# Kernel optimization log

Measured on AMD Instinct MI355X. Metric: run time of the kernel, lower is better.

Reference implementation:

```python
import jax, jax.numpy as jnp
import numpy as np

B = 8192
G, K, D = 8, 1024, 64  # num_codebooks, codebook_size, code_dim
INIT_SCALE = 0.1


def setup_inputs() -> dict:
    key = jax.random.key(0)
    kz, kc = jax.random.split(key)
    z = jax.random.normal(kz, (B, G * D), dtype=jnp.float32)
    codebook = jax.random.uniform(kc, (G, K, D), dtype=jnp.float32,
                                  minval=-INIT_SCALE, maxval=INIT_SCALE)
    return {"z": z, "codebook": codebook}


def reference(z, codebook):
    # Eval-mode forward of GroupedVectorQuantizer (no EMA buffer mutation).
    b = z.shape[0]
    g, k, d = codebook.shape
    zg = z.reshape(b, g, d)                       # [B,G,D]
    # squared L2 distance via ||z||^2 + ||c||^2 - 2 z.c (avoids [B,G,K,D] diff tensor)
    z2 = jnp.sum(zg * zg, axis=-1, keepdims=True)           # [B,G,1]
    c2 = jnp.sum(codebook * codebook, axis=-1)[None]        # [1,G,K]
    zc = jnp.einsum('bgd,gkd->bgk', zg, codebook)           # [B,G,K]
    dist = z2 + c2 - 2.0 * zc                               # [B,G,K]
    indices = jnp.argmin(dist, axis=-1)                     # [B,G] int32
    # gather nearest codes per group
    zq = codebook[jnp.arange(g)[None, :], indices]          # [B,G,D]
    commitment_loss = jnp.mean((zg - jax.lax.stop_gradient(zq)) ** 2)
    codebook_loss = jnp.zeros((), dtype=z.dtype)
    # straight-through estimator
    z_st = zg + jax.lax.stop_gradient(zq - zg)
    quantized_flat = z_st.reshape(b, g * d)
    # codebook usage entropy / perplexity (pooled over batch and groups, as in torch)
    usage = jnp.zeros((k,), dtype=jnp.float32).at[indices.reshape(-1)].add(1.0) / (b * g)
    entropy = -jnp.sum(usage * jnp.log(usage + 1e-10))
    perplexity = jnp.exp(entropy)
    return quantized_flat, indices, commitment_loss, codebook_loss, entropy, perplexity
```

## Files before the change

kernel.cpp:

```cpp
#include <hip/hip_runtime.h>
#include <hip/hip_bf16.h>
#include <math.h>

#define NB 8192
#define NG 8
#define NK 1024
#define ND 64
#define GD 512
#define MARGIN 2.5e-4f

typedef __attribute__((ext_vector_type(8))) short short8;
typedef __attribute__((ext_vector_type(4))) float f32x4;

#define WS_C2_OFF   0
#define WS_STG_OFF  32768
#define WS_HIST_OFF (32768 + 2097152 + 1048576)
#define WS_PART_OFF (WS_HIST_OFF + 4096)

typedef const __attribute__((address_space(1))) unsigned int glds_src_t;
typedef __attribute__((address_space(3))) unsigned int glds_dst_t;

__device__ inline void bsplit(float v, short& hs, short& ls) {
    __hip_bfloat16 h = __float2bfloat16(v);
    float hf = __bfloat162float(h);
    __hip_bfloat16 l = __float2bfloat16(v - hf);
    hs = *reinterpret_cast<short*>(&h);
    ls = *reinterpret_cast<short*>(&l);
}

__device__ inline float wredsum(float v) {
#pragma unroll
    for (int st = 1; st < 64; st <<= 1) v += __shfl_xor(v, st);
    return v;
}

__global__ __launch_bounds__(64) void vq_prep(const float* __restrict__ cb,
                                              float* __restrict__ ws) {
    const int gid = blockIdx.x * 64 + threadIdx.x;
    const int g  = gid >> 10, k = gid & 1023;
    const int it = k >> 6,   row = k & 63;
    const float* c = cb + (size_t)gid * ND;
    char* base = (char*)ws + WS_STG_OFF + (size_t)(g * 16 + it) * 16384 + row * 128;

    float a0 = 0.f, a1 = 0.f, a2 = 0.f, a3 = 0.f;
#pragma unroll
    for (int j = 0; j < 8; ++j) {
        const float4 v0 = reinterpret_cast<const float4*>(c)[2 * j];
        const float4 v1 = reinterpret_cast<const float4*>(c)[2 * j + 1];
        a0 = fmaf(v0.x, v0.x, a0); a1 = fmaf(v0.y, v0.y, a1);
        a2 = fmaf(v0.z, v0.z, a2); a3 = fmaf(v0.w, v0.w, a3);
        a0 = fmaf(v1.x, v1.x, a0); a1 = fmaf(v1.y, v1.y, a1);
        a2 = fmaf(v1.z, v1.z, a2); a3 = fmaf(v1.w, v1.w, a3);
        short h0, l0, h1, l1, h2, l2, h3, l3;
        short h4, l4, h5, l5, h6, l6, h7, l7;
        bsplit(v0.x, h0, l0); bsplit(v0.y, h1, l1);
        bsplit(v0.z, h2, l2); bsplit(v0.w, h3, l3);
        bsplit(v1.x, h4, l4); bsplit(v1.y, h5, l5);
        bsplit(v1.z, h6, l6); bsplit(v1.w, h7, l7);
        short8 hs, ls;
        hs[0] = h0; hs[1] = h1; hs[2] = h2; hs[3] = h3;
        hs[4] = h4; hs[5] = h5; hs[6] = h6; hs[7] = h7;
        ls[0] = l0; ls[1] = l1; ls[2] = l2; ls[3] = l3;
        ls[4] = l4; ls[5] = l5; ls[6] = l6; ls[7] = l7;
        const int off = (j ^ (row & 7)) << 4;
        *reinterpret_cast<short8*>(base + off)        = hs;
        *reinterpret_cast<short8*>(base + 8192 + off) = ls;
    }
    ((float*)((char*)ws + WS_C2_OFF))[gid] = (a0 + a1) + (a2 + a3);
    if (gid < NK) ((unsigned*)((char*)ws + WS_HIST_OFF))[gid] = 0u;
}

__global__ __launch_bounds__(256, 2) void vq_score(const float* __restrict__ z,
                                                   const float* __restrict__ cb,
                                                   float* __restrict__ out,
                                                   float* __restrict__ ws) {
    __shared__ __align__(16) char smem[2][32768];
    __shared__ int winfo[4][32];
    const int tid  = threadIdx.x;
    const int w    = tid >> 6;
    const int lane = tid & 63;
    const int lo   = lane & 15, hi = lane >> 4;
    const int g    = blockIdx.y;
    const int rbase = blockIdx.x * 128 + w * 32;

    const char*  stg = (const char*)ws + WS_STG_OFF + (size_t)g * 16 * 16384;
    const float* c2g = (const float*)((const char*)ws + WS_C2_OFF) + g * NK;

    short8 Ah[2][2], Al[2][2];
#pragma unroll
    for (int m = 0; m < 2; ++m)
#pragma unroll
        for (int ks = 0; ks < 2; ++ks) {
            const float* zp = z + (size_t)(rbase + m * 16 + lo) * GD + g * ND + ks * 32 + hi * 8;
            float vv[8];
            *reinterpret_cast<float4*>(&vv[0]) = reinterpret_cast<const float4*>(zp)[0];
            *reinterpret_cast<float4*>(&vv[4]) = reinterpret_cast<const float4*>(zp)[1];
#pragma unroll
            for (int e = 0; e < 8; ++e) {
                short hs, ls;
                bsplit(vv[e], hs, ls);
                Ah[m][ks][e] = hs;
                Al[m][ks][e] = ls;
            }
        }

    float best[8], b2[8];
    int   bk[8], k2[8];
#pragma unroll
    for (int s = 0; s < 8; ++s) { best[s] = 3.0e38f; b2[s] = 3.0e38f; bk[s] = 0; k2[s] = 0; }

    const int rowoff = lo * 128;
    const int swz0 = ((hi ^ (lo & 7)) << 4);
    const int swz1 = (((4 + hi) ^ (lo & 7)) << 4);
    char* lds0 = &smem[0][0];

    const char* src = stg;
    auto STAGE = [&](const char* s, unsigned dOff) {
#pragma unroll
        for (int i = 0; i < 8; ++i) {
            const int so = (i >> 2) * 16384 + w * 4096 + (i & 3) * 1024 + lane * 16;
            __builtin_amdgcn_global_load_lds(
                (glds_src_t*)(const void*)(s + so),
                (glds_dst_t*)(void*)(lds0 + dOff + so), 16, 0, 0);
        }
    };

    STAGE(src, 0u);
    src += 32768;
    __syncthreads();

#pragma unroll 1
    for (int it = 0; it < 8; ++it) {
        float c2v[2][4];
#pragma unroll
        for (int t = 0; t < 2; ++t)
#pragma unroll
            for (int n = 0; n < 4; ++n)
                c2v[t][n] = c2g[it * 128 + t * 64 + n * 16 + lo];

        const unsigned cur = (unsigned)(it & 1) * 32768u;
        if (it < 7) { STAGE(src, cur ^ 32768u); src += 32768; }

        const char* bufc = lds0 + cur;
#pragma unroll
        for (int t = 0; t < 2; ++t) {
            f32x4 acc[2][4] = {};
#pragma unroll
            for (int ks = 0; ks < 2; ++ks) {
                short8 bh[4], bl[4];
#pragma unroll
                for (int n = 0; n < 4; ++n) {
                    const int off = t * 16384 + n * 2048 + rowoff + (ks ? swz1 : swz0);
                    bh[n] = *reinterpret_cast<const short8*>(bufc + off);
                    bl[n] = *reinterpret_cast<const short8*>(bufc + 8192 + off);
                }
#pragma unroll
                for (int n = 0; n < 4; ++n)
#pragma unroll
                    for (int m = 0; m < 2; ++m)
                        acc[m][n] = __builtin_amdgcn_mfma_f32_16x16x32_bf16(
                            ks ? Ah[m][1] : Ah[m][0], bh[n], acc[m][n], 0, 0, 0);
#pragma unroll
                for (int n = 0; n < 4; ++n)
#pragma unroll
                    for (int m = 0; m < 2; ++m)
                        acc[m][n] = __builtin_amdgcn_mfma_f32_16x16x32_bf16(
                            ks ? Ah[m][1] : Ah[m][0], bl[n], acc[m][n], 0, 0, 0);
#pragma unroll
                for (int n = 0; n < 4; ++n)
#pragma unroll
                    for (int m = 0; m < 2; ++m)
                        acc[m][n] = __builtin_amdgcn_mfma_f32_16x16x32_bf16(
                            ks ? Al[m][1] : Al[m][0], bh[n], acc[m][n], 0, 0, 0);
            }

#pragma unroll
            for (int n = 0; n < 4; ++n) {
                const int kv = it * 128 + t * 64 + n * 16 + lo;
#pragma unroll
                for (int m = 0; m < 2; ++m)
#pragma unroll
                    for (int q = 0; q < 4; ++q) {
                        const int sidx = m * 4 + q;
                        const float s = fmaf(-2.0f, acc[m][n][q], c2v[t][n]);
                        const bool lt  = s < best[sidx];
                        const bool lt2 = s < b2[sidx];
                        b2[sidx]   = lt ? best[sidx] : (lt2 ? s : b2[sidx]);
                        k2[sidx]   = lt ? bk[sidx]   : (lt2 ? kv : k2[sidx]);
                        best[sidx] = lt ? s : best[sidx];
                        bk[sidx]   = lt ? kv : bk[sidx];
                    }
            }
        }
        __syncthreads();
    }

#pragma unroll
    for (int s = 0; s < 8; ++s) {
        const int m = s >> 2, q = s & 3;
        float pb = best[s], p2 = b2[s];
        int   kq = bk[s],   kq2 = k2[s];
#pragma unroll
        for (int st = 1; st < 16; st <<= 1) {
            const float ob  = __shfl_xor(pb, st);
            const int   obk = __shfl_xor(kq, st);
            const float ob2 = __shfl_xor(p2, st);
            const int   ok2 = __shfl_xor(kq2, st);
            const bool bet = (ob < pb) || (ob == pb && obk < kq);
            const float lb  = bet ? pb : ob;
            const int   lk  = bet ? kq : obk;
            const float wb2 = bet ? ob2 : p2;
            const int   wk2 = bet ? ok2 : kq2;
            const bool s2 = (lb < wb2) || (lb == wb2 && lk < wk2);
            p2  = s2 ? lb : wb2;
            kq2 = s2 ? lk : wk2;
            pb  = bet ? ob : pb;
            kq  = bet ? obk : kq;
        }
        if (lo == 0) {
            const int ridx = m * 16 + hi * 4 + q;
            const bool fl = (p2 - pb) <= MARGIN;
            winfo[w][ridx] = kq | (kq2 << 10) | (fl ? (1 << 20) : 0);
        }
    }
    asm volatile("s_waitcnt lgkmcnt(0)" ::: "memory");
    __builtin_amdgcn_sched_barrier(0);

    float zrow[32];
    {
        const float* zbase = z + (size_t)rbase * GD + g * ND + lane;
#pragma unroll
        for (int r = 0; r < 32; ++r) zrow[r] = zbase[(size_t)r * GD];
    }
    const float* cgrp = cb + (size_t)g * NK * ND;
    int* wif = &winfo[w][0];
    float esum = 0.f;

#pragma unroll 4
    for (int r = 0; r < 32; ++r) {
        const int info = wif[r];
        const float zd = zrow[r];
        int win = info & 1023;

        if (info & (1 << 20)) {
            const int kalt = (info >> 10) & 1023;
            const float z2 = wredsum(zd * zd);
            const float c1 = cgrp[(size_t)win * ND + lane];
            const float d1 = (z2 + c2g[win]) - 2.0f * wredsum(zd * c1);
            const float c2 = cgrp[(size_t)kalt * ND + lane];
            const float d2 = (z2 + c2g[kalt]) - 2.0f * wredsum(zd * c2);
            if (d2 < d1 || (d2 == d1 && kalt < win)) win = kalt;
            if (lane == 0) wif[r] = win;
        }

        const float cw = cgrp[(size_t)win * ND + lane];
        out[(size_t)(rbase + r) * GD + g * ND + lane] = zd + (cw - zd);
        const float e = zd - cw;
        esum += e * e;
    }

    asm volatile("s_waitcnt lgkmcnt(0)" ::: "memory");
    __builtin_amdgcn_sched_barrier(0);
    if (lane < 32) {
        const int wv = wif[lane] & 1023;
        out[(size_t)NB * GD + (size_t)(rbase + lane) * NG + g] = (float)wv;
        atomicAdd((unsigned*)((char*)ws + WS_HIST_OFF) + wv, 1u);
    }

    esum = wredsum(esum);
    __shared__ float sh[4];
    if (lane == 0) sh[w] = esum;
    __syncthreads();
    if (tid == 0)
        ((float*)((char*)ws + WS_PART_OFF))[blockIdx.y * 64 + blockIdx.x] =
            (sh[0] + sh[1]) + (sh[2] + sh[3]);
}

__global__ __launch_bounds__(1024) void vq_final(const float* __restrict__ ws,
                                                 float* __restrict__ out) {
    const int t = threadIdx.x;
    __shared__ float se[1024];
    __shared__ float sc[1024];
    const unsigned cnt = ((const unsigned*)((const char*)ws + WS_HIST_OFF))[t];
    const float usage = (float)cnt * (1.0f / 65536.f);
    se[t] = -usage * logf(usage + 1e-10f);
    const float* part = (const float*)((const char*)ws + WS_PART_OFF);
    sc[t] = (t < 512) ? part[t] : 0.f;
    __syncthreads();
    for (int st = 512; st > 0; st >>= 1) {
        if (t < st) {
            se[t] += se[t + st];
            sc[t] += sc[t + st];
        }
        __syncthreads();
    }
    if (t == 0) {
        float* scal = out + (size_t)NB * GD + (size_t)NB * NG;
        scal[0] = sc[0] * (1.0f / ((float)NB * NG * ND));
        scal[1] = 0.0f;
        scal[2] = se[0];
        scal[3] = expf(se[0]);
    }
}

extern "C" void kernel_launch(void* const* d_in, const int* in_sizes, int n_in,
                              void* d_out, int out_size, void* d_ws, size_t ws_size,
                              hipStream_t stream) {
    const float* z  = (const float*)d_in[0];
    const float* cb = (const float*)d_in[1];
    float* out = (float*)d_out;
    float* ws  = (float*)d_ws;

    hipLaunchKernelGGL(vq_prep,  dim3(128),   dim3(64),   0, stream, cb, ws);
    hipLaunchKernelGGL(vq_score, dim3(64, 8), dim3(256),  0, stream, z, cb, out, ws);
    hipLaunchKernelGGL(vq_final, dim3(1),     dim3(1024), 0, stream, ws, out);
}
```

Before: 69.19 us.

## Halve rows per wave and codebook stage size to double block count and occupancy

Each wave now handles 16 rows instead of 32, and the codebook is staged in 16 KB chunks over 16 iterations instead of 32 KB over 8. The grid doubles to 128x8 blocks, launch bounds allow 4 blocks per CU, and the z row preload into 32 registers is replaced by per-row loads. The aim is to cut register and LDS pressure so more waves run and the 512-block grid's tail on 256 CUs goes away. In exchange, each block stages the full per-group codebook for half as many rows, so codebook traffic per row doubles and MFMA reuse of B operands halves.

After: 58.91 us. -14.9%, faster.

```diff
diff --git a/kernel.cpp b/kernel.cpp
--- a/kernel.cpp
+++ b/kernel.cpp
@@ -70,44 +70,42 @@
     if (gid < NK) ((unsigned*)((char*)ws + WS_HIST_OFF))[gid] = 0u;
 }
 
-__global__ __launch_bounds__(256, 2) void vq_score(const float* __restrict__ z,
+__global__ __launch_bounds__(256, 4) void vq_score(const float* __restrict__ z,
                                                    const float* __restrict__ cb,
                                                    float* __restrict__ out,
                                                    float* __restrict__ ws) {
-    __shared__ __align__(16) char smem[2][32768];
-    __shared__ int winfo[4][32];
+    __shared__ __align__(16) char smem[2][16384];
+    __shared__ int winfo[4][16];
     const int tid  = threadIdx.x;
     const int w    = tid >> 6;
     const int lane = tid & 63;
     const int lo   = lane & 15, hi = lane >> 4;
     const int g    = blockIdx.y;
-    const int rbase = blockIdx.x * 128 + w * 32;
+    const int rbase = blockIdx.x * 64 + w * 16;
 
     const char*  stg = (const char*)ws + WS_STG_OFF + (size_t)g * 16 * 16384;
     const float* c2g = (const float*)((const char*)ws + WS_C2_OFF) + g * NK;
 
-    short8 Ah[2][2], Al[2][2];
-#pragma unroll
-    for (int m = 0; m < 2; ++m)
-#pragma unroll
-        for (int ks = 0; ks < 2; ++ks) {
-            const float* zp = z + (size_t)(rbase + m * 16 + lo) * GD + g * ND + ks * 32 + hi * 8;
-            float vv[8];
-            *reinterpret_cast<float4*>(&vv[0]) = reinterpret_cast<const float4*>(zp)[0];
-            *reinterpret_cast<float4*>(&vv[4]) = reinterpret_cast<const float4*>(zp)[1];
-#pragma unroll
-            for (int e = 0; e < 8; ++e) {
-                short hs, ls;
-                bsplit(vv[e], hs, ls);
-                Ah[m][ks][e] = hs;
-                Al[m][ks][e] = ls;
-            }
-        }
-
-    float best[8], b2[8];
-    int   bk[8], k2[8];
-#pragma unroll
-    for (int s = 0; s < 8; ++s) { best[s] = 3.0e38f; b2[s] = 3.0e38f; bk[s] = 0; k2[s] = 0; }
+    short8 Ah[2], Al[2];
+#pragma unroll
+    for (int ks = 0; ks < 2; ++ks) {
+        const float* zp = z + (size_t)(rbase + lo) * GD + g * ND + ks * 32 + hi * 8;
+        float vv[8];
+        *reinterpret_cast<float4*>(&vv[0]) = reinterpret_cast<const float4*>(zp)[0];
+        *reinterpret_cast<float4*>(&vv[4]) = reinterpret_cast<const float4*>(zp)[1];
+#pragma unroll
+        for (int e = 0; e < 8; ++e) {
+            short hs, ls;
+            bsplit(vv[e], hs, ls);
+            Ah[ks][e] = hs;
+            Al[ks][e] = ls;
+        }
+    }
+
+    float best[4], b2[4];
+    int   bk[4], k2[4];
+#pragma unroll
+    for (int q = 0; q < 4; ++q) { best[q] = 3.0e38f; b2[q] = 3.0e38f; bk[q] = 0; k2[q] = 0; }
 
     const int rowoff = lo * 128;
     const int swz0 = ((hi ^ (lo & 7)) << 4);
@@ -117,8 +115,8 @@
     const char* src = stg;
     auto STAGE = [&](const char* s, unsigned dOff) {
 #pragma unroll
-        for (int i = 0; i < 8; ++i) {
-            const int so = (i >> 2) * 16384 + w * 4096 + (i & 3) * 1024 + lane * 16;
+        for (int i = 0; i < 4; ++i) {
+            const int so = w * 4096 + i * 1024 + lane * 16;
             __builtin_amdgcn_global_load_lds(
                 (glds_src_t*)(const void*)(s + so),
                 (glds_dst_t*)(void*)(lds0 + dOff + so), 16, 0, 0);
@@ -126,80 +124,65 @@
     };
 
     STAGE(src, 0u);
-    src += 32768;
+    src += 16384;
     __syncthreads();
 
 #pragma unroll 1
-    for (int it = 0; it < 8; ++it) {
-        float c2v[2][4];
-#pragma unroll
-        for (int t = 0; t < 2; ++t)
+    for (int it = 0; it < 16; ++it) {
+        const int kb = it * 64;
+        float c2v[4];
+#pragma unroll
+        for (int n = 0; n < 4; ++n) c2v[n] = c2g[kb + n * 16 + lo];
+
+        const unsigned cur = (unsigned)(it & 1) * 16384u;
+        if (it < 15) { STAGE(src, cur ^ 16384u); src += 16384; }
+
+        const char* bufc = lds0 + cur;
+        f32x4 acc[4] = {{0.f,0.f,0.f,0.f},{0.f,0.f,0.f,0.f},{0.f,0.f,0.f,0.f},{0.f,0.f,0.f,0.f}};
+#pragma unroll
+        for (int ks = 0; ks < 2; ++ks) {
+            short8 bh[4], bl[4];
+#pragma unroll
+            for (int n = 0; n < 4; ++n) {
+                const int off = n * 2048 + rowoff + (ks ? swz1 : swz0);
+                bh[n] = *reinterpret_cast<const short8*>(bufc + off);
+                bl[n] = *reinterpret_cast<const short8*>(bufc + 8192 + off);
+            }
 #pragma unroll
             for (int n = 0; n < 4; ++n)
-                c2v[t][n] = c2g[it * 128 + t * 64 + n * 16 + lo];
-
-        const unsigned cur = (unsigned)(it & 1) * 32768u;
-        if (it < 7) { STAGE(src, cur ^ 32768u); src += 32768; }
-
-        const char* bufc = lds0 + cur;
-#pragma unroll
-        for (int t = 0; t < 2; ++t) {
-            f32x4 acc[2][4] = {};
-#pragma unroll
-            for (int ks = 0; ks < 2; ++ks) {
-                short8 bh[4], bl[4];
-#pragma unroll
-                for (int n = 0; n < 4; ++n) {
-                    const int off = t * 16384 + n * 2048 + rowoff + (ks ? swz1 : swz0);
-                    bh[n] = *reinterpret_cast<const short8*>(bufc + off);
-                    bl[n] = *reinterpret_cast<const short8*>(bufc + 8192 + off);
-                }
-#pragma unroll
-                for (int n = 0; n < 4; ++n)
-#pragma unroll
-                    for (int m = 0; m < 2; ++m)
-                        acc[m][n] = __builtin_amdgcn_mfma_f32_16x16x32_bf16(
-                            ks ? Ah[m][1] : Ah[m][0], bh[n], acc[m][n], 0, 0, 0);
-#pragma unroll
-                for (int n = 0; n < 4; ++n)
-#pragma unroll
-                    for (int m = 0; m < 2; ++m)
-                        acc[m][n] = __builtin_amdgcn_mfma_f32_16x16x32_bf16(
-                            ks ? Ah[m][1] : Ah[m][0], bl[n], acc[m][n], 0, 0, 0);
-#pragma unroll
-                for (int n = 0; n < 4; ++n)
-#pragma unroll
-                    for (int m = 0; m < 2; ++m)
-                        acc[m][n] = __builtin_amdgcn_mfma_f32_16x16x32_bf16(
-                            ks ? Al[m][1] : Al[m][0], bh[n], acc[m][n], 0, 0, 0);
+                acc[n] = __builtin_amdgcn_mfma_f32_16x16x32_bf16(
+                    ks ? Ah[1] : Ah[0], bh[n], acc[n], 0, 0, 0);
+#pragma unroll
+            for (int n = 0; n < 4; ++n)
+                acc[n] = __builtin_amdgcn_mfma_f32_16x16x32_bf16(
+                    ks ? Ah[1] : Ah[0], bl[n], acc[n], 0, 0, 0);
+#pragma unroll
+            for (int n = 0; n < 4; ++n)
+                acc[n] = __builtin_amdgcn_mfma_f32_16x16x32_bf16(
+                    ks ? Al[1] : Al[0], bh[n], acc[n], 0, 0, 0);
+        }
+
+#pragma unroll
+        for (int n = 0; n < 4; ++n) {
+            const int kv = kb + n * 16 + lo;
+#pragma unroll
+            for (int q = 0; q < 4; ++q) {
+                const float s = fmaf(-2.0f, acc[n][q], c2v[n]);
+                const bool lt  = s < best[q];
+                const bool lt2 = s < b2[q];
+                b2[q]   = lt ? best[q] : (lt2 ? s : b2[q]);
+                k2[q]   = lt ? bk[q]   : (lt2 ? kv : k2[q]);
+                best[q] = lt ? s : best[q];
+                bk[q]   = lt ? kv : bk[q];
             }
-
-#pragma unroll
-            for (int n = 0; n < 4; ++n) {
-                const int kv = it * 128 + t * 64 + n * 16 + lo;
-#pragma unroll
-                for (int m = 0; m < 2; ++m)
-#pragma unroll
-                    for (int q = 0; q < 4; ++q) {
-                        const int sidx = m * 4 + q;
-                        const float s = fmaf(-2.0f, acc[m][n][q], c2v[t][n]);
-                        const bool lt  = s < best[sidx];
-                        const bool lt2 = s < b2[sidx];
-                        b2[sidx]   = lt ? best[sidx] : (lt2 ? s : b2[sidx]);
-                        k2[sidx]   = lt ? bk[sidx]   : (lt2 ? kv : k2[sidx]);
-                        best[sidx] = lt ? s : best[sidx];
-                        bk[sidx]   = lt ? kv : bk[sidx];
-                    }
-            }
         }
         __syncthreads();
     }
 
 #pragma unroll
-    for (int s = 0; s < 8; ++s) {
-        const int m = s >> 2, q = s & 3;
-        float pb = best[s], p2 = b2[s];
-        int   kq = bk[s],   kq2 = k2[s];
+    for (int q = 0; q < 4; ++q) {
+        float pb = best[q], p2 = b2[q];
+        int   kq = bk[q],   kq2 = k2[q];
 #pragma unroll
         for (int st = 1; st < 16; st <<= 1) {
             const float ob  = __shfl_xor(pb, st);
@@ -218,7 +201,7 @@
             kq  = bet ? obk : kq;
         }
         if (lo == 0) {
-            const int ridx = m * 16 + hi * 4 + q;
+            const int ridx = hi * 4 + q;
             const bool fl = (p2 - pb) <= MARGIN;
             winfo[w][ridx] = kq | (kq2 << 10) | (fl ? (1 << 20) : 0);
         }
@@ -226,20 +209,14 @@
     asm volatile("s_waitcnt lgkmcnt(0)" ::: "memory");
     __builtin_amdgcn_sched_barrier(0);
 
-    float zrow[32];
-    {
-        const float* zbase = z + (size_t)rbase * GD + g * ND + lane;
-#pragma unroll
-        for (int r = 0; r < 32; ++r) zrow[r] = zbase[(size_t)r * GD];
-    }
     const float* cgrp = cb + (size_t)g * NK * ND;
     int* wif = &winfo[w][0];
     float esum = 0.f;
-
-#pragma unroll 4
-    for (int r = 0; r < 32; ++r) {
+#pragma unroll 1
+    for (int r = 0; r < 16; ++r) {
         const int info = wif[r];
-        const float zd = zrow[r];
+        const int row  = rbase + r;
+        const float zd = z[(size_t)row * GD + g * ND + lane];
         int win = info & 1023;
 
         if (info & (1 << 20)) {
@@ -254,14 +231,14 @@
         }
 
         const float cw = cgrp[(size_t)win * ND + lane];
-        out[(size_t)(rbase + r) * GD + g * ND + lane] = zd + (cw - zd);
+        out[(size_t)row * GD + g * ND + lane] = zd + (cw - zd);
         const float e = zd - cw;
         esum += e * e;
     }
 
     asm volatile("s_waitcnt lgkmcnt(0)" ::: "memory");
     __builtin_amdgcn_sched_barrier(0);
-    if (lane < 32) {
+    if (lane < 16) {
         const int wv = wif[lane] & 1023;
         out[(size_t)NB * GD + (size_t)(rbase + lane) * NG + g] = (float)wv;
         atomicAdd((unsigned*)((char*)ws + WS_HIST_OFF) + wv, 1u);
@@ -272,7 +249,7 @@
     if (lane == 0) sh[w] = esum;
     __syncthreads();
     if (tid == 0)
-        ((float*)((char*)ws + WS_PART_OFF))[blockIdx.y * 64 + blockIdx.x] =
+        ((float*)((char*)ws + WS_PART_OFF))[blockIdx.y * 128 + blockIdx.x] =
             (sh[0] + sh[1]) + (sh[2] + sh[3]);
 }
 
@@ -285,7 +262,7 @@
     const float usage = (float)cnt * (1.0f / 65536.f);
     se[t] = -usage * logf(usage + 1e-10f);
     const float* part = (const float*)((const char*)ws + WS_PART_OFF);
-    sc[t] = (t < 512) ? part[t] : 0.f;
+    sc[t] = part[t];
     __syncthreads();
     for (int st = 512; st > 0; st >>= 1) {
         if (t < st) {
@@ -311,7 +288,7 @@
     float* out = (float*)d_out;
     float* ws  = (float*)d_ws;
 
-    hipLaunchKernelGGL(vq_prep,  dim3(128),   dim3(64),   0, stream, cb, ws);
-    hipLaunchKernelGGL(vq_score, dim3(64, 8), dim3(256),  0, stream, z, cb, out, ws);
-    hipLaunchKernelGGL(vq_final, dim3(1),     dim3(1024), 0, stream, ws, out);
-}
+    hipLaunchKernelGGL(vq_prep,  dim3(128),    dim3(64),   0, stream, cb, ws);
+    hipLaunchKernelGGL(vq_score, dim3(128, 8), dim3(256),  0, stream, z, cb, out, ws);
+    hipLaunchKernelGGL(vq_final, dim3(1),      dim3(1024), 0, stream, ws, out);
+}
```
